# Kernel optimization log

Hardware: AMD Instinct MI355X
Metric: run time of the kernel (lower is better)

## Reference

```python
import jax, jax.numpy as jnp
import numpy as np

NUM_HEADS = 16


def setup_inputs() -> dict:
    key = jax.random.key(0)
    ks = jax.random.split(key, 6)
    B, N, M, C = 2, 2048, 2048, 1024
    return {
        "reference_data": jax.random.normal(ks[0], (B, N, C), dtype=jnp.float32),
        "target_data": jax.random.normal(ks[1], (B, M, C), dtype=jnp.float32),
        "Wq": jax.random.normal(ks[2], (C, C), dtype=jnp.float32) * (C ** -0.5),
        "Wkv": jax.random.normal(ks[3], (C, 2 * C), dtype=jnp.float32) * (C ** -0.5),
        "Wproj": jax.random.normal(ks[4], (C, C), dtype=jnp.float32) * (C ** -0.5),
        "bproj": jnp.zeros((C,), dtype=jnp.float32),
    }


def reference(reference_data, target_data, Wq, Wkv, Wproj, bproj):
    B, N, C = reference_data.shape
    M = target_data.shape[1]
    H = NUM_HEADS
    hd = C // H
    scale = hd ** -0.5
    # k, v from reference: [B, N, 2, H, hd] -> two [B, H, N, hd]
    kv = (reference_data @ Wkv).reshape(B, N, 2, H, hd)
    k = jnp.transpose(kv[:, :, 0], (0, 2, 1, 3))  # [B,H,N,hd]
    v = jnp.transpose(kv[:, :, 1], (0, 2, 1, 3))  # [B,H,N,hd]
    # q from target: [B, H, M, hd]
    q = jnp.transpose((target_data @ Wq).reshape(B, M, H, hd), (0, 2, 1, 3))
    attn = jnp.einsum("bhid,bhjd->bhij", q, k) * scale  # [B,H,M,N]
    attn = jax.nn.softmax(attn, axis=-1)
    x = jnp.einsum("bhij,bhjd->bhid", attn, v)  # [B,H,M,hd]
    x = jnp.transpose(x, (0, 2, 1, 3)).reshape(B, M, C)
    return x @ Wproj + bproj
```

## Files before the change

kernel.cpp:

```cpp
#include <hip/hip_runtime.h>
#include <hip/hip_bf16.h>
#include <stdint.h>

#define SEQ   2048
#define CH    1024
#define NH    16
#define HD    64

typedef short bf8 __attribute__((ext_vector_type(8)));
typedef short bf4 __attribute__((ext_vector_type(4)));
typedef float f4  __attribute__((ext_vector_type(4)));
typedef unsigned short u16;

#define GAS(p) ((const __attribute__((address_space(1))) void*)(p))
#define LAS(p) ((__attribute__((address_space(3))) void*)(p))

__device__ __forceinline__ u16 f2bf(float f) {
  uint32_t u = __float_as_uint(f);
  u += 0x7fffu + ((u >> 16) & 1u);
  return (u16)(u >> 16);
}

__device__ __forceinline__ uint32_t pk2bf(float a, float b) {
  float2 f; f.x = a; f.y = b;
  __hip_bfloat162 h = __float22bfloat162_rn(f);
  union { __hip_bfloat162 h; uint32_t u; } cv; cv.h = h;
  return cv.u;
}

__device__ __forceinline__ float fexp2(float x) {
#if __has_builtin(__builtin_amdgcn_exp2f)
  return __builtin_amdgcn_exp2f(x);
#else
  return exp2f(x);
#endif
}

__device__ __forceinline__ f4 MFMA32(bf8 a, bf8 b, f4 c) {
  return __builtin_amdgcn_mfma_f32_16x16x32_bf16(a, b, c, 0, 0, 0);
}

__device__ __forceinline__ f4 MFMA16(bf4 a, bf4 b, f4 c) {
#if __has_builtin(__builtin_amdgcn_mfma_f32_16x16x16_bf16)
  return __builtin_amdgcn_mfma_f32_16x16x16_bf16(a, b, c, 0, 0, 0);
#elif __has_builtin(__builtin_amdgcn_mfma_f32_16x16x16bf16_1k)
  return __builtin_amdgcn_mfma_f32_16x16x16bf16_1k(a, b, c, 0, 0, 0);
#else
  f4 d = c;
  asm volatile("v_mfma_f32_16x16x16_bf16 %0, %1, %2, %0"
               : "+v"(d) : "v"(a), "v"(b));
  return d;
#endif
}

__device__ __forceinline__ int xcd_swz(int f, int cpx) {
  return (f & 7) * cpx + (f >> 3);
}

__global__ void prep(const float* __restrict__ ref, u16* __restrict__ refb,
                     const float* __restrict__ tgt, u16* __restrict__ tgtb,
                     const float* __restrict__ Wq, u16* __restrict__ Wqt,
                     const float* __restrict__ Wkv, u16* __restrict__ Wkvt,
                     const float* __restrict__ Wp, u16* __restrict__ Wpt) {
  __shared__ float tile[32][33];
  int blk = blockIdx.x;
  int t = threadIdx.x;
  if (blk < 8192) {
    const float* in; u16* out;
    if (blk < 4096) { in = ref; out = refb; } else { in = tgt; out = tgtb; blk -= 4096; }
    int i = (blk * 256 + t) * 4;
    float4 f = *reinterpret_cast<const float4*>(in + i);
    ushort4 o;
    o.x = f2bf(f.x); o.y = f2bf(f.y); o.z = f2bf(f.z); o.w = f2bf(f.w);
    *reinterpret_cast<ushort4*>(out + i) = o;
    return;
  }
  blk -= 8192;
  int x = blk & 127, by = blk >> 7;
  const float* in; u16* out; int N;
  if (x < 32)       { in = Wq;  out = Wqt;  N = CH;     }
  else if (x < 96)  { in = Wkv; out = Wkvt; N = 2 * CH; x -= 32; }
  else              { in = Wp;  out = Wpt;  N = CH;     x -= 96; }
  const int K = CH;
  int bn = x * 32, bk = by * 32;
  int tx = t & 31, ty = t >> 5;
  #pragma unroll
  for (int i = ty; i < 32; i += 8)
    tile[i][tx] = in[(size_t)(bk + i) * N + bn + tx];
  __syncthreads();
  #pragma unroll
  for (int i = ty; i < 32; i += 8)
    out[(size_t)(bn + i) * K + bk + tx] = f2bf(tile[tx][i]);
}

__global__ __launch_bounds__(256, 3)
void gemm_qkv(const u16* __restrict__ tgtb, const u16* __restrict__ refb,
              const u16* __restrict__ Wqt, const u16* __restrict__ Wkvt,
              u16* __restrict__ qb, u16* __restrict__ karr, u16* __restrict__ varr)
{
  __shared__ __align__(16) u16 As[2][4096];
  __shared__ __align__(16) u16 Bs[2][4096];
  const int tid = threadIdx.x;
  const int lane = tid & 63, wave = tid >> 6;
  const int l16 = lane & 15, q = lane >> 4;
  const int tflat = xcd_swz(blockIdx.y * 24 + blockIdx.x, 96);
  const int bx = tflat % 24, by = tflat / 24;
  const bool isQ = bx >= 16;
  const u16* A  = isQ ? tgtb : refb;
  const u16* Bt = isQ ? Wqt : Wkvt;
  const int n0 = (isQ ? (bx - 16) : bx) * 128;
  const int m0 = by * 128;
  const int wm = (wave >> 1) * 64, wn = (wave & 1) * 64;
  const int Kdim = CH;
  const int c = tid, c2 = tid + 256;
  const int ar = c >> 2, ac = (c & 3) << 3, ar2 = c2 >> 2, ac2 = (c2 & 3) << 3;

  f4 acc[4][4] = {};

  #define STAGE_G(buf, k0)                                                      \
    { __builtin_amdgcn_global_load_lds(                                         \
          GAS(&A[(size_t)(m0 + ar) * Kdim + (k0) + ac]),                        \
          LAS(&As[buf][c << 3]), 16, 0, 0);                                     \
      __builtin_amdgcn_global_load_lds(                                         \
          GAS(&A[(size_t)(m0 + ar2) * Kdim + (k0) + ac2]),                      \
          LAS(&As[buf][c2 << 3]), 16, 0, 0);                                    \
      __builtin_amdgcn_global_load_lds(                                         \
          GAS(&Bt[(size_t)(n0 + ar) * Kdim + (k0) + ac]),                       \
          LAS(&Bs[buf][c << 3]), 16, 0, 0);                                     \
      __builtin_amdgcn_global_load_lds(                                         \
          GAS(&Bt[(size_t)(n0 + ar2) * Kdim + (k0) + ac2]),                     \
          LAS(&Bs[buf][c2 << 3]), 16, 0, 0); }

  STAGE_G(0, 0);
  for (int kk = 0; kk < 32; ++kk) {
    __syncthreads();
    if (kk < 31) STAGE_G((kk + 1) & 1, (kk + 1) * 32);
    const u16* as = As[kk & 1];
    const u16* bs = Bs[kk & 1];
    bf8 a[4], b[4];
    #pragma unroll
    for (int i = 0; i < 4; ++i)
      a[i] = *reinterpret_cast<const bf8*>(&as[(wm + i * 16 + l16) * 32 + q * 8]);
    #pragma unroll
    for (int j = 0; j < 4; ++j)
      b[j] = *reinterpret_cast<const bf8*>(&bs[(wn + j * 16 + l16) * 32 + q * 8]);
    #pragma unroll
    for (int i = 0; i < 4; ++i)
      #pragma unroll
      for (int j = 0; j < 4; ++j)
        acc[i][j] = MFMA32(a[i], b[j], acc[i][j]);
  }
  #undef STAGE_G

  #pragma unroll
  for (int i = 0; i < 4; ++i) {
    const int mbase = m0 + wm + i * 16 + q * 4;
    const int b = mbase >> 11, ns0 = mbase & (SEQ - 1);
    #pragma unroll
    for (int j = 0; j < 4; ++j) {
      const int n = n0 + wn + j * 16 + l16;
      if (isQ) {
        int h = n >> 6, d = n & 63;
        #pragma unroll
        for (int r = 0; r < 4; ++r)
          qb[(size_t)((b * NH + h) * SEQ + ns0 + r) * HD + d] =
              f2bf(acc[i][j][r] * 0.1803368801f);
      } else if (n < CH) {
        int h = n >> 6, d = n & 63;
        size_t base = (size_t)(b * NH + h) * SEQ * HD;
        int off = (((ns0 >> 4) * 2 + (d >> 5)) * 4 + ((d >> 3) & 3)) * 128
                  + (d & 7);
        #pragma unroll
        for (int r = 0; r < 4; ++r)
          karr[base + off + ((ns0 + r) & 15) * 8] = f2bf(acc[i][j][r]);
      } else {
        int c2v = n - CH, h = c2v >> 6, d = c2v & 63;
        size_t base = (size_t)(b * NH + h) * SEQ * HD;
        int off = (((ns0 >> 4) * 2 + (d >> 5)) * 4 + ((ns0 >> 2) & 3)) * 128
                  + (d & 15) * 8 + ((d >> 4) & 1) * 4;
        ushort4 st;
        st.x = f2bf(acc[i][j][0]); st.y = f2bf(acc[i][j][1]);
        st.z = f2bf(acc[i][j][2]); st.w = f2bf(acc[i][j][3]);
        *reinterpret_cast<ushort4*>(&varr[base + off]) = st;
      }
    }
  }
}

__global__ __launch_bounds__(256, 2)
void gemm_proj(const u16* __restrict__ A, const u16* __restrict__ Bt,
               float* __restrict__ fo, const float* __restrict__ bias)
{
  __shared__ __align__(16) u16 As[2][2048];
  __shared__ __align__(16) u16 Bs[2][4096];
  const int tid = threadIdx.x;
  const int lane = tid & 63, wave = tid >> 6;
  const int l16 = lane & 15, q = lane >> 4;
  const int tflat = xcd_swz(blockIdx.y * 8 + blockIdx.x, 64);
  const int m0 = (tflat / 8) * 64, n0 = (tflat % 8) * 128;
  const int wm = (wave >> 1) * 32, wn = (wave & 1) * 64;
  const int Kdim = CH;
  const int c = tid, c2 = tid + 256;
  const int ar = c >> 2, ac = (c & 3) << 3, ar2 = c2 >> 2, ac2 = (c2 & 3) << 3;

  f4 acc[2][4] = {};

  const int aar = c >> 2;
  const int aac = (c & 3) << 3;
  #define STAGE_P(buf, k0)                                                      \
    { __builtin_amdgcn_global_load_lds(                                         \
          GAS(&A[(size_t)(m0 + aar) * Kdim + (k0) + aac]),                      \
          LAS(&As[buf][c << 3]), 16, 0, 0);                                     \
      __builtin_amdgcn_global_load_lds(                                         \
          GAS(&Bt[(size_t)(n0 + ar) * Kdim + (k0) + ac]),                       \
          LAS(&Bs[buf][c << 3]), 16, 0, 0);                                     \
      __builtin_amdgcn_global_load_lds(                                         \
          GAS(&Bt[(size_t)(n0 + ar2) * Kdim + (k0) + ac2]),                     \
          LAS(&Bs[buf][c2 << 3]), 16, 0, 0); }

  STAGE_P(0, 0);
  for (int kk = 0; kk < 32; ++kk) {
    __syncthreads();
    if (kk < 31) STAGE_P((kk + 1) & 1, (kk + 1) * 32);
    const u16* as = As[kk & 1];
    const u16* bs = Bs[kk & 1];
    bf8 a[2], b[4];
    #pragma unroll
    for (int i = 0; i < 2; ++i)
      a[i] = *reinterpret_cast<const bf8*>(&as[(wm + i * 16 + l16) * 32 + q * 8]);
    #pragma unroll
    for (int j = 0; j < 4; ++j)
      b[j] = *reinterpret_cast<const bf8*>(&bs[(wn + j * 16 + l16) * 32 + q * 8]);
    #pragma unroll
    for (int i = 0; i < 2; ++i)
      #pragma unroll
      for (int j = 0; j < 4; ++j)
        acc[i][j] = MFMA32(a[i], b[j], acc[i][j]);
  }
  #undef STAGE_P

  #pragma unroll
  for (int i = 0; i < 2; ++i) {
    const int mbase = m0 + wm + i * 16 + q * 4;
    #pragma unroll
    for (int j = 0; j < 4; ++j) {
      const int n = n0 + wn + j * 16 + l16;
      #pragma unroll
      for (int r = 0; r < 4; ++r)
        fo[(size_t)(mbase + r) * CH + n] = acc[i][j][r] + bias[n];
    }
  }
}

__global__ __launch_bounds__(256, 4)
void attn(const u16* __restrict__ Q, const u16* __restrict__ Karr,
          const u16* __restrict__ Varr, u16* __restrict__ X)
{
  __shared__ __align__(16) u16 Ks[2][4096];
  __shared__ __align__(16) u16 Vs[2][4096];
  const int tid = threadIdx.x;
  const int lane = tid & 63;
  const int l16 = lane & 15, q = lane >> 4;
  const int tflat = xcd_swz(blockIdx.y * 32 + blockIdx.x, 128);
  const int bh = tflat / 32;
  const int m0 = (tflat % 32) * 64;
  const int wm = (tid >> 6) * 16;

  const u16* Qb = Q    + (size_t)bh * SEQ * HD;
  const u16* Kb = Karr + (size_t)bh * SEQ * HD;
  const u16* Vb = Varr + (size_t)bh * SEQ * HD;

  bf8 qf[2];
  #pragma unroll
  for (int s = 0; s < 2; ++s)
    qf[s] = *reinterpret_cast<const bf8*>(
        &Qb[(size_t)(m0 + wm + l16) * HD + s * 32 + q * 8]);

  const short one_bf = 0x3F80;
  const bf4 ones = {one_bf, one_bf, one_bf, one_bf};

  f4 o[4] = {};
  f4 ds = {};

  #define STAGE_A(buf, t)                                                      \
    { __builtin_amdgcn_global_load_lds(GAS(Kb + (size_t)(t) * 4096 + tid * 8), \
                                       LAS(&Ks[buf][tid * 8]), 16, 0, 0);      \
      __builtin_amdgcn_global_load_lds(GAS(Kb + (size_t)(t) * 4096 + 2048 + tid * 8), \
                                       LAS(&Ks[buf][2048 + tid * 8]), 16, 0, 0); \
      __builtin_amdgcn_global_load_lds(GAS(Vb + (size_t)(t) * 4096 + tid * 8), \
                                       LAS(&Vs[buf][tid * 8]), 16, 0, 0);      \
      __builtin_amdgcn_global_load_lds(GAS(Vb + (size_t)(t) * 4096 + 2048 + tid * 8), \
                                       LAS(&Vs[buf][2048 + tid * 8]), 16, 0, 0); }

  STAGE_A(0, 0);
  for (int t = 0; t < 32; ++t) {
    __syncthreads();
    if (t < 31) STAGE_A((t + 1) & 1, t + 1);
    const u16* ks = Ks[t & 1];
    const u16* vs = Vs[t & 1];

    bf4 pa[4];
    #pragma unroll
    for (int j = 0; j < 4; ++j) {
      bf8 kf0 = *reinterpret_cast<const bf8*>(&ks[((j * 2 + 0) * 4 + q) * 128 + l16 * 8]);
      bf8 kf1 = *reinterpret_cast<const bf8*>(&ks[((j * 2 + 1) * 4 + q) * 128 + l16 * 8]);
      f4 zf = {};
      zf = MFMA32(kf0, qf[0], zf);
      zf = MFMA32(kf1, qf[1], zf);
      union { bf4 v; uint32_t u[2]; } w;
      w.u[0] = pk2bf(fexp2(zf[0]), fexp2(zf[1]));
      w.u[1] = pk2bf(fexp2(zf[2]), fexp2(zf[3]));
      pa[j] = w.v;
    }

    #pragma unroll
    for (int j = 0; j < 4; ++j) {
      ds = MFMA16(pa[j], ones, ds);
      #pragma unroll
      for (int dh = 0; dh < 2; ++dh) {
        bf8 vv = *reinterpret_cast<const bf8*>(&vs[((j * 2 + dh) * 4 + q) * 128 + l16 * 8]);
        bf4 v0 = __builtin_shufflevector(vv, vv, 0, 1, 2, 3);
        bf4 v1 = __builtin_shufflevector(vv, vv, 4, 5, 6, 7);
        o[dh * 2 + 0] = MFMA16(pa[j], v0, o[dh * 2 + 0]);
        o[dh * 2 + 1] = MFMA16(pa[j], v1, o[dh * 2 + 1]);
      }
    }
  }
  #undef STAGE_A

  const int b = bh >> 4, h = bh & (NH - 1);
  #pragma unroll
  for (int r = 0; r < 4; ++r) {
    float ir = 1.0f / ds[r];
    int m = m0 + wm + q * 4 + r;
    #pragma unroll
    for (int dt = 0; dt < 4; ++dt) {
      int d = dt * 16 + l16;
      X[(size_t)(b * SEQ + m) * CH + h * HD + d] = f2bf(o[dt][r] * ir);
    }
  }
}

extern "C" void kernel_launch(void* const* d_in, const int* in_sizes, int n_in,
                              void* d_out, int out_size, void* d_ws, size_t ws_size,
                              hipStream_t stream) {
  const float* ref   = (const float*)d_in[0];
  const float* tgt   = (const float*)d_in[1];
  const float* Wq    = (const float*)d_in[2];
  const float* Wkv   = (const float*)d_in[3];
  const float* Wproj = (const float*)d_in[4];
  const float* bproj = (const float*)d_in[5];
  float* out = (float*)d_out;

  char* ws = (char*)d_ws;
  u16* refb = (u16*)(ws);
  u16* tgtb = (u16*)(ws + (8  << 20));
  u16* Wqt  = (u16*)(ws + (16 << 20));
  u16* Wkvt = (u16*)(ws + (18 << 20));
  u16* Wpt  = (u16*)(ws + (22 << 20));
  u16* qb   = (u16*)(ws + (24 << 20));
  u16* karr = (u16*)(ws + (32 << 20));
  u16* varr = (u16*)(ws + (40 << 20));
  u16* xb   = (u16*)(ws + (48 << 20));

  prep<<<12288, 256, 0, stream>>>(ref, refb, tgt, tgtb, Wq, Wqt, Wkv, Wkvt, Wproj, Wpt);

  gemm_qkv<<<dim3(24, 32), 256, 0, stream>>>(tgtb, refb, Wqt, Wkvt, qb, karr, varr);

  attn<<<dim3(32, 32), 256, 0, stream>>>(qb, karr, varr, xb);

  gemm_proj<<<dim3(8, 64), 256, 0, stream>>>(xb, Wpt, out, bproj);
}
```

Baseline: 203.1 us.

## Fuse fp32-to-bf16 activation conversion into QKV GEMM A-tile loads

Removes the separate elementwise pass that converted the reference and target activations to bf16, so the QKV GEMM now reads fp32 activations directly. The A tiles are loaded into registers, converted and packed to bf16, then written to shared memory after the MFMA work of the current step, which keeps the software prefetch overlap. This avoids writing and re-reading 16 MB of bf16 activations. In exchange, each A tile is re-read as fp32 from global memory by every column block (doubling its bytes), and register pressure and VALU work inside the GEMM loop go up.

```diff
diff --git a/kernel.cpp b/kernel.cpp
--- a/kernel.cpp
+++ b/kernel.cpp
@@ -57,25 +57,12 @@
   return (f & 7) * cpx + (f >> 3);
 }
 
-__global__ void prep(const float* __restrict__ ref, u16* __restrict__ refb,
-                     const float* __restrict__ tgt, u16* __restrict__ tgtb,
-                     const float* __restrict__ Wq, u16* __restrict__ Wqt,
+__global__ void prep(const float* __restrict__ Wq, u16* __restrict__ Wqt,
                      const float* __restrict__ Wkv, u16* __restrict__ Wkvt,
                      const float* __restrict__ Wp, u16* __restrict__ Wpt) {
   __shared__ float tile[32][33];
   int blk = blockIdx.x;
   int t = threadIdx.x;
-  if (blk < 8192) {
-    const float* in; u16* out;
-    if (blk < 4096) { in = ref; out = refb; } else { in = tgt; out = tgtb; blk -= 4096; }
-    int i = (blk * 256 + t) * 4;
-    float4 f = *reinterpret_cast<const float4*>(in + i);
-    ushort4 o;
-    o.x = f2bf(f.x); o.y = f2bf(f.y); o.z = f2bf(f.z); o.w = f2bf(f.w);
-    *reinterpret_cast<ushort4*>(out + i) = o;
-    return;
-  }
-  blk -= 8192;
   int x = blk & 127, by = blk >> 7;
   const float* in; u16* out; int N;
   if (x < 32)       { in = Wq;  out = Wqt;  N = CH;     }
@@ -94,7 +81,7 @@
 }
 
 __global__ __launch_bounds__(256, 3)
-void gemm_qkv(const u16* __restrict__ tgtb, const u16* __restrict__ refb,
+void gemm_qkv(const float* __restrict__ tgtf, const float* __restrict__ reff,
               const u16* __restrict__ Wqt, const u16* __restrict__ Wkvt,
               u16* __restrict__ qb, u16* __restrict__ karr, u16* __restrict__ varr)
 {
@@ -106,7 +93,7 @@
   const int tflat = xcd_swz(blockIdx.y * 24 + blockIdx.x, 96);
   const int bx = tflat % 24, by = tflat / 24;
   const bool isQ = bx >= 16;
-  const u16* A  = isQ ? tgtb : refb;
+  const float* Af = isQ ? tgtf : reff;
   const u16* Bt = isQ ? Wqt : Wkvt;
   const int n0 = (isQ ? (bx - 16) : bx) * 128;
   const int m0 = by * 128;
@@ -117,24 +104,37 @@
 
   f4 acc[4][4] = {};
 
-  #define STAGE_G(buf, k0)                                                      \
+  #define STAGE_B(buf, k0)                                                      \
     { __builtin_amdgcn_global_load_lds(                                         \
-          GAS(&A[(size_t)(m0 + ar) * Kdim + (k0) + ac]),                        \
-          LAS(&As[buf][c << 3]), 16, 0, 0);                                     \
-      __builtin_amdgcn_global_load_lds(                                         \
-          GAS(&A[(size_t)(m0 + ar2) * Kdim + (k0) + ac2]),                      \
-          LAS(&As[buf][c2 << 3]), 16, 0, 0);                                    \
-      __builtin_amdgcn_global_load_lds(                                         \
           GAS(&Bt[(size_t)(n0 + ar) * Kdim + (k0) + ac]),                       \
           LAS(&Bs[buf][c << 3]), 16, 0, 0);                                     \
       __builtin_amdgcn_global_load_lds(                                         \
           GAS(&Bt[(size_t)(n0 + ar2) * Kdim + (k0) + ac2]),                     \
           LAS(&Bs[buf][c2 << 3]), 16, 0, 0); }
 
-  STAGE_G(0, 0);
+  #define ISSUE_A(k0)                                                           \
+    fa0 = *reinterpret_cast<const float4*>(&Af[(size_t)(m0 + ar) * Kdim + (k0) + ac]);      \
+    fa1 = *reinterpret_cast<const float4*>(&Af[(size_t)(m0 + ar) * Kdim + (k0) + ac + 4]);  \
+    fb0 = *reinterpret_cast<const float4*>(&Af[(size_t)(m0 + ar2) * Kdim + (k0) + ac2]);    \
+    fb1 = *reinterpret_cast<const float4*>(&Af[(size_t)(m0 + ar2) * Kdim + (k0) + ac2 + 4]);
+
+  #define WRITE_A(buf)                                                          \
+    { union { bf8 v; uint32_t u[4]; } wa;                                       \
+      wa.u[0] = pk2bf(fa0.x, fa0.y); wa.u[1] = pk2bf(fa0.z, fa0.w);             \
+      wa.u[2] = pk2bf(fa1.x, fa1.y); wa.u[3] = pk2bf(fa1.z, fa1.w);             \
+      *reinterpret_cast<bf8*>(&As[buf][c << 3]) = wa.v;                         \
+      wa.u[0] = pk2bf(fb0.x, fb0.y); wa.u[1] = pk2bf(fb0.z, fb0.w);             \
+      wa.u[2] = pk2bf(fb1.x, fb1.y); wa.u[3] = pk2bf(fb1.z, fb1.w);             \
+      *reinterpret_cast<bf8*>(&As[buf][c2 << 3]) = wa.v; }
+
+  float4 fa0, fa1, fb0, fb1;
+
+  ISSUE_A(0);
+  STAGE_B(0, 0);
+  WRITE_A(0);
   for (int kk = 0; kk < 32; ++kk) {
     __syncthreads();
-    if (kk < 31) STAGE_G((kk + 1) & 1, (kk + 1) * 32);
+    if (kk < 31) { ISSUE_A((kk + 1) * 32); STAGE_B((kk + 1) & 1, (kk + 1) * 32); }
     const u16* as = As[kk & 1];
     const u16* bs = Bs[kk & 1];
     bf8 a[4], b[4];
@@ -149,8 +149,11 @@
       #pragma unroll
       for (int j = 0; j < 4; ++j)
         acc[i][j] = MFMA32(a[i], b[j], acc[i][j]);
-  }
-  #undef STAGE_G
+    if (kk < 31) WRITE_A((kk + 1) & 1);
+  }
+  #undef STAGE_B
+  #undef ISSUE_A
+  #undef WRITE_A
 
   #pragma unroll
   for (int i = 0; i < 4; ++i) {
@@ -353,8 +356,6 @@
   float* out = (float*)d_out;
 
   char* ws = (char*)d_ws;
-  u16* refb = (u16*)(ws);
-  u16* tgtb = (u16*)(ws + (8  << 20));
   u16* Wqt  = (u16*)(ws + (16 << 20));
   u16* Wkvt = (u16*)(ws + (18 << 20));
   u16* Wpt  = (u16*)(ws + (22 << 20));
@@ -363,9 +364,9 @@
   u16* varr = (u16*)(ws + (40 << 20));
   u16* xb   = (u16*)(ws + (48 << 20));
 
-  prep<<<12288, 256, 0, stream>>>(ref, refb, tgt, tgtb, Wq, Wqt, Wkv, Wkvt, Wproj, Wpt);
-
-  gemm_qkv<<<dim3(24, 32), 256, 0, stream>>>(tgtb, refb, Wqt, Wkvt, qb, karr, varr);
+  prep<<<4096, 256, 0, stream>>>(Wq, Wqt, Wkv, Wkvt, Wproj, Wpt);
+
+  gemm_qkv<<<dim3(24, 32), 256, 0, stream>>>(tgt, ref, Wqt, Wkvt, qb, karr, varr);
 
   attn<<<dim3(32, 32), 256, 0, stream>>>(qb, karr, varr, xb);
 
```

Measured after the change: 216.0 us. 1.06x slower.
